# Performance work log

Measured on AMD Instinct MI355X. Metric: run time of the kernel, lower is better.

Reference implementation:

```python
import jax, jax.numpy as jnp
import numpy as np

H = 1024
V = 50257


def setup_inputs() -> dict:
    key = jax.random.key(0)
    ks = jax.random.split(key, 10)
    s = 0.02
    return {
        "x": jax.random.randint(ks[0], (1,), 0, V, dtype=jnp.int32),
        "h0": jax.random.normal(ks[1], (1, 1, H), jnp.float32),
        "c0": jax.random.normal(ks[2], (1, 1, H), jnp.float32),
        "emb": jax.random.normal(ks[3], (V, H), jnp.float32) * s,
        "w_ih": jax.random.normal(ks[4], (4 * H, H), jnp.float32) * s,
        "w_hh": jax.random.normal(ks[5], (4 * H, H), jnp.float32) * s,
        "b_ih": jax.random.normal(ks[6], (4 * H,), jnp.float32) * s,
        "b_hh": jax.random.normal(ks[7], (4 * H,), jnp.float32) * s,
        "w_out": jax.random.normal(ks[8], (V, H), jnp.float32) * s,
        "b_out": jax.random.normal(ks[9], (V,), jnp.float32) * s,
    }


def reference(x, h0, c0, emb, w_ih, w_hh, b_ih, b_hh, w_out, b_out):
    # embedding lookup + view(1,1,-1) + relu -> [1, H]
    e = jax.nn.relu(emb[x].reshape(1, H))
    h = h0[0]  # [1, H]
    c = c0[0]  # [1, H]
    # single LSTM cell step; PyTorch gate order: i, f, g, o
    gates = e @ w_ih.T + b_ih + h @ w_hh.T + b_hh  # [1, 4H]
    i, f, g, o = jnp.split(gates, 4, axis=1)
    c_new = jax.nn.sigmoid(f) * c + jax.nn.sigmoid(i) * jnp.tanh(g)
    h_new = jax.nn.sigmoid(o) * jnp.tanh(c_new)
    # output projection + log-softmax over vocab
    logits = h_new @ w_out.T + b_out  # [1, V]
    out = jax.nn.log_softmax(logits, axis=1)
    return out, (h_new[None, :, :], c_new[None, :, :])
```

## Files before the change

### kernel.cpp

```cpp
#include <hip/hip_runtime.h>
#include <math.h>

#define HH 1024
#define VV 50257
#define NLB 1024
#define NEXTRA 1105

__device__ __forceinline__ void lse_comb(float& m, float& s, float om, float os) {
    float M = fmaxf(m, om);
    s = s * __expf(m - M) + os * __expf(om - M);
    m = M;
}

__device__ __forceinline__ float sigmoidf(float x) { return 1.0f / (1.0f + __expf(-x)); }

__device__ __forceinline__ float dot4(float4 a, float4 b) {
    return a.x * b.x + a.y * b.y + a.z * b.z + a.w * b.w;
}

__global__ __launch_bounds__(512) void k_gatecell(
    const int* __restrict__ x, const float* __restrict__ emb,
    const float* __restrict__ h0, const float* __restrict__ c0,
    const float* __restrict__ w_ih, const float* __restrict__ w_hh,
    const float* __restrict__ b_ih, const float* __restrict__ b_hh,
    float* __restrict__ out) {
    __shared__ float sg2[8];
    const int j = blockIdx.x;
    const int w = threadIdx.x >> 6;
    const int lane = threadIdx.x & 63;
    const int g = w >> 1, hf = w & 1;
    const int row = g * HH + j;
    const int base = hf * 512 + lane * 8;

    const float* e  = emb + (size_t)x[0] * HH + base;
    const float* wi = w_ih + (size_t)row * HH + base;
    const float* wh = w_hh + (size_t)row * HH + base;
    const float* hp = h0 + base;

    float4 wi0 = *reinterpret_cast<const float4*>(wi);
    float4 wi1 = *reinterpret_cast<const float4*>(wi + 4);
    float4 wh0 = *reinterpret_cast<const float4*>(wh);
    float4 wh1 = *reinterpret_cast<const float4*>(wh + 4);
    float4 e0  = *reinterpret_cast<const float4*>(e);
    float4 e1  = *reinterpret_cast<const float4*>(e + 4);
    float4 hv0 = *reinterpret_cast<const float4*>(hp);
    float4 hv1 = *reinterpret_cast<const float4*>(hp + 4);
    e0.x = fmaxf(e0.x, 0.f); e0.y = fmaxf(e0.y, 0.f);
    e0.z = fmaxf(e0.z, 0.f); e0.w = fmaxf(e0.w, 0.f);
    e1.x = fmaxf(e1.x, 0.f); e1.y = fmaxf(e1.y, 0.f);
    e1.z = fmaxf(e1.z, 0.f); e1.w = fmaxf(e1.w, 0.f);

    float acc = dot4(wi0, e0) + dot4(wi1, e1) + dot4(wh0, hv0) + dot4(wh1, hv1);
#pragma unroll
    for (int off = 1; off < 64; off <<= 1) acc += __shfl_xor(acc, off, 64);
    if (lane == 0)
        sg2[w] = acc + (hf == 0 ? b_ih[row] + b_hh[row] : 0.0f);
    __syncthreads();
    if (threadIdx.x == 0) {
        float ig = sigmoidf(sg2[0] + sg2[1]);
        float fg = sigmoidf(sg2[2] + sg2[3]);
        float gg = tanhf(sg2[4] + sg2[5]);
        float og = sigmoidf(sg2[6] + sg2[7]);
        float c = fg * c0[j] + ig * gg;
        float h = og * tanhf(c);
        out[VV + j] = h;
        out[VV + HH + j] = c;
    }
}

__global__ __launch_bounds__(256, 4) void k_logits_lse(
    const float* __restrict__ w_out, const float* __restrict__ b_out,
    const float* __restrict__ h, float* __restrict__ logits,
    float* __restrict__ pm, float* __restrict__ ps) {
    __shared__ float4 hs[256];
    __shared__ float sm[4], ss[4];
    const int tid = threadIdx.x;
    const int w = tid >> 6;
    const int lane = tid & 63;

    hs[tid] = reinterpret_cast<const float4*>(h)[tid];
    __syncthreads();

    const int wid = blockIdx.x * 4 + w;
    const bool extra = (wid < NEXTRA);
    const int base = wid * 12 + (extra ? wid : NEXTRA);
    const float* wp = w_out + (size_t)base * HH + lane * 4;

    float4 A[3][4], B[3][4], T[4];

#pragma unroll
    for (int p = 0; p < 2; ++p) {
        const float* pa = wp + (size_t)(2 * p) * HH;
        const float* pb = pa + HH;
#pragma unroll
        for (int c = 0; c < 4; ++c) {
            A[p][c] = *reinterpret_cast<const float4*>(pa + c * 256);
            B[p][c] = *reinterpret_cast<const float4*>(pb + c * 256);
        }
    }

    float m = -1e30f, s = 0.0f;
#pragma unroll
    for (int k = 0; k < 6; ++k) {
        if (k < 4) {
            const int sl = (k + 2) % 3;
            const float* pa = wp + (size_t)(2 * (k + 2)) * HH;
            const float* pb = pa + HH;
#pragma unroll
            for (int c = 0; c < 4; ++c) {
                A[sl][c] = *reinterpret_cast<const float4*>(pa + c * 256);
                B[sl][c] = *reinterpret_cast<const float4*>(pb + c * 256);
            }
        } else if (k == 4 && extra) {
            const float* pt = wp + (size_t)12 * HH;
#pragma unroll
            for (int c = 0; c < 4; ++c)
                T[c] = *reinterpret_cast<const float4*>(pt + c * 256);
        }
        const int cs = k % 3;
        float accA = 0.0f, accB = 0.0f;
#pragma unroll
        for (int c = 0; c < 4; ++c) {
            float4 hc = hs[lane + c * 64];
            accA += dot4(A[cs][c], hc);
            accB += dot4(B[cs][c], hc);
        }
#pragma unroll
        for (int off = 1; off < 64; off <<= 1) {
            accA += __shfl_xor(accA, off, 64);
            accB += __shfl_xor(accB, off, 64);
        }
        const int rA = base + 2 * k;
        const float vA = accA + b_out[rA];
        const float vB = accB + b_out[rA + 1];
        if (lane == 0) {
            logits[rA] = vA;
            logits[rA + 1] = vB;
        }
        float M = fmaxf(m, vA);
        s = s * __expf(m - M) + __expf(vA - M);
        m = M;
        M = fmaxf(m, vB);
        s = s * __expf(m - M) + __expf(vB - M);
        m = M;
    }
    if (extra) {
        float acc = 0.0f;
#pragma unroll
        for (int c = 0; c < 4; ++c) {
            float4 hc = hs[lane + c * 64];
            acc += dot4(T[c], hc);
        }
#pragma unroll
        for (int off = 1; off < 64; off <<= 1) acc += __shfl_xor(acc, off, 64);
        const int r = base + 12;
        const float v = acc + b_out[r];
        if (lane == 0) logits[r] = v;
        float M = fmaxf(m, v);
        s = s * __expf(m - M) + __expf(v - M);
        m = M;
    }

    if (lane == 0) { sm[w] = m; ss[w] = s; }
    __syncthreads();
    if (tid == 0) {
        float M = sm[0], S = ss[0];
#pragma unroll
        for (int q = 1; q < 4; ++q) lse_comb(M, S, sm[q], ss[q]);
        pm[blockIdx.x] = M;
        ps[blockIdx.x] = S;
    }
}

__global__ __launch_bounds__(256) void k_final(
    const float* __restrict__ logits, const float* __restrict__ pm,
    const float* __restrict__ ps, float* __restrict__ out) {
    __shared__ float sm[4], ss[4];
    __shared__ float sZ;
    int tid = threadIdx.x;
    int lane = tid & 63;
    float m = -1e30f, s = 0.0f;
#pragma unroll
    for (int t = 0; t < NLB / 256; ++t) {
        int p = tid + t * 256;
        lse_comb(m, s, pm[p], ps[p]);
    }
#pragma unroll
    for (int off = 1; off < 64; off <<= 1) {
        float om = __shfl_xor(m, off, 64);
        float os = __shfl_xor(s, off, 64);
        lse_comb(m, s, om, os);
    }
    if (lane == 0) { sm[tid >> 6] = m; ss[tid >> 6] = s; }
    __syncthreads();
    if (tid == 0) {
        float M = sm[0], S = ss[0];
#pragma unroll
        for (int q = 1; q < 4; ++q) lse_comb(M, S, sm[q], ss[q]);
        sZ = M + logf(S);
    }
    __syncthreads();
    float Z = sZ;
    for (int i = blockIdx.x * 256 + tid; i < VV; i += gridDim.x * 256)
        out[i] = logits[i] - Z;
}

extern "C" void kernel_launch(void* const* d_in, const int* in_sizes, int n_in,
                              void* d_out, int out_size, void* d_ws, size_t ws_size,
                              hipStream_t stream) {
    const int*   x     = (const int*)d_in[0];
    const float* h0    = (const float*)d_in[1];
    const float* c0    = (const float*)d_in[2];
    const float* emb   = (const float*)d_in[3];
    const float* w_ih  = (const float*)d_in[4];
    const float* w_hh  = (const float*)d_in[5];
    const float* b_ih  = (const float*)d_in[6];
    const float* b_hh  = (const float*)d_in[7];
    const float* w_out = (const float*)d_in[8];
    const float* b_out = (const float*)d_in[9];
    float* out = (float*)d_out;
    float* ws  = (float*)d_ws;

    float* logits = ws;
    float* pm     = ws + 50304;
    float* ps     = pm + NLB;

    k_gatecell<<<HH, 512, 0, stream>>>(x, emb, h0, c0, w_ih, w_hh, b_ih, b_hh, out);
    k_logits_lse<<<NLB, 256, 0, stream>>>(w_out, b_out, out + VV, logits, pm, ps);
    k_final<<<256, 256, 0, stream>>>(logits, pm, ps, out);
}
```

Before: 50.40 us.

## Interleave logits rows across waves and double grid for more occupancy

Doubles the number of logits blocks and assigns rows to waves with a grid-wide stride instead of contiguous chunks of 12-13 rows. Each wave now loads its two rows per step on demand, replacing the three-stage register prefetch ring. Launch bounds rise to 8 blocks per CU so more waves are in flight to hide memory latency. The tradeoff is less per-wave prefetch depth in exchange for higher occupancy, and the final reduction kernel now combines twice as many partials.

```diff
diff --git a/kernel.cpp b/kernel.cpp
--- a/kernel.cpp
+++ b/kernel.cpp
@@ -3,8 +3,9 @@
 
 #define HH 1024
 #define VV 50257
-#define NLB 1024
-#define NEXTRA 1105
+#define NLB 2048
+#define NWAVE (NLB * 4)
+#define NTAIL (VV - 6 * NWAVE)
 
 __device__ __forceinline__ void lse_comb(float& m, float& s, float om, float os) {
     float M = fmaxf(m, om);
@@ -68,7 +69,7 @@
     }
 }
 
-__global__ __launch_bounds__(256, 4) void k_logits_lse(
+__global__ __launch_bounds__(256, 8) void k_logits_lse(
     const float* __restrict__ w_out, const float* __restrict__ b_out,
     const float* __restrict__ h, float* __restrict__ logits,
     float* __restrict__ pm, float* __restrict__ ps) {
@@ -82,60 +83,38 @@
     __syncthreads();
 
     const int wid = blockIdx.x * 4 + w;
-    const bool extra = (wid < NEXTRA);
-    const int base = wid * 12 + (extra ? wid : NEXTRA);
-    const float* wp = w_out + (size_t)base * HH + lane * 4;
-
-    float4 A[3][4], B[3][4], T[4];
-
-#pragma unroll
-    for (int p = 0; p < 2; ++p) {
-        const float* pa = wp + (size_t)(2 * p) * HH;
-        const float* pb = pa + HH;
-#pragma unroll
-        for (int c = 0; c < 4; ++c) {
-            A[p][c] = *reinterpret_cast<const float4*>(pa + c * 256);
-            B[p][c] = *reinterpret_cast<const float4*>(pb + c * 256);
-        }
-    }
-
+    const float* wb = w_out + (size_t)wid * HH + lane * 4;
     float m = -1e30f, s = 0.0f;
-#pragma unroll
-    for (int k = 0; k < 6; ++k) {
-        if (k < 4) {
-            const int sl = (k + 2) % 3;
-            const float* pa = wp + (size_t)(2 * (k + 2)) * HH;
-            const float* pb = pa + HH;
-#pragma unroll
-            for (int c = 0; c < 4; ++c) {
-                A[sl][c] = *reinterpret_cast<const float4*>(pa + c * 256);
-                B[sl][c] = *reinterpret_cast<const float4*>(pb + c * 256);
-            }
-        } else if (k == 4 && extra) {
-            const float* pt = wp + (size_t)12 * HH;
-#pragma unroll
-            for (int c = 0; c < 4; ++c)
-                T[c] = *reinterpret_cast<const float4*>(pt + c * 256);
-        }
-        const int cs = k % 3;
-        float accA = 0.0f, accB = 0.0f;
-#pragma unroll
-        for (int c = 0; c < 4; ++c) {
-            float4 hc = hs[lane + c * 64];
-            accA += dot4(A[cs][c], hc);
-            accB += dot4(B[cs][c], hc);
-        }
+
+#pragma unroll
+    for (int k = 0; k < 3; ++k) {
+        const int cA = 2 * k, cB = 2 * k + 1;
+        const float* pa = wb + (size_t)cA * NWAVE * HH;
+        const float* pb = wb + (size_t)cB * NWAVE * HH;
+        float4 a0 = *reinterpret_cast<const float4*>(pa);
+        float4 a1 = *reinterpret_cast<const float4*>(pa + 256);
+        float4 a2 = *reinterpret_cast<const float4*>(pa + 512);
+        float4 a3 = *reinterpret_cast<const float4*>(pa + 768);
+        float4 b0 = *reinterpret_cast<const float4*>(pb);
+        float4 b1 = *reinterpret_cast<const float4*>(pb + 256);
+        float4 b2 = *reinterpret_cast<const float4*>(pb + 512);
+        float4 b3 = *reinterpret_cast<const float4*>(pb + 768);
+        float accA = dot4(a0, hs[lane]) + dot4(a1, hs[lane + 64]) +
+                     dot4(a2, hs[lane + 128]) + dot4(a3, hs[lane + 192]);
+        float accB = dot4(b0, hs[lane]) + dot4(b1, hs[lane + 64]) +
+                     dot4(b2, hs[lane + 128]) + dot4(b3, hs[lane + 192]);
 #pragma unroll
         for (int off = 1; off < 64; off <<= 1) {
             accA += __shfl_xor(accA, off, 64);
             accB += __shfl_xor(accB, off, 64);
         }
-        const int rA = base + 2 * k;
+        const int rA = wid + cA * NWAVE;
+        const int rB = wid + cB * NWAVE;
         const float vA = accA + b_out[rA];
-        const float vB = accB + b_out[rA + 1];
+        const float vB = accB + b_out[rB];
         if (lane == 0) {
             logits[rA] = vA;
-            logits[rA + 1] = vB;
+            logits[rB] = vB;
         }
         float M = fmaxf(m, vA);
         s = s * __expf(m - M) + __expf(vA - M);
@@ -144,16 +123,17 @@
         s = s * __expf(m - M) + __expf(vB - M);
         m = M;
     }
-    if (extra) {
-        float acc = 0.0f;
-#pragma unroll
-        for (int c = 0; c < 4; ++c) {
-            float4 hc = hs[lane + c * 64];
-            acc += dot4(T[c], hc);
-        }
+    if (wid < NTAIL) {
+        const float* pt = wb + (size_t)6 * NWAVE * HH;
+        float4 t0 = *reinterpret_cast<const float4*>(pt);
+        float4 t1 = *reinterpret_cast<const float4*>(pt + 256);
+        float4 t2 = *reinterpret_cast<const float4*>(pt + 512);
+        float4 t3 = *reinterpret_cast<const float4*>(pt + 768);
+        float acc = dot4(t0, hs[lane]) + dot4(t1, hs[lane + 64]) +
+                    dot4(t2, hs[lane + 128]) + dot4(t3, hs[lane + 192]);
 #pragma unroll
         for (int off = 1; off < 64; off <<= 1) acc += __shfl_xor(acc, off, 64);
-        const int r = base + 12;
+        const int r = wid + 6 * NWAVE;
         const float v = acc + b_out[r];
         if (lane == 0) logits[r] = v;
         float M = fmaxf(m, v);
```

After: 46.08 us. 1.09x faster.
